# Kernel tuning notes

Hardware: AMD Instinct MI355X
Metric: run time of the kernel (lower is better)

Reference implementation:

```python
import jax, jax.numpy as jnp
import numpy as np

B, T, D, N, L = 8, 2048, 256, 64, 4
LN_EPS = 1e-5


def setup_inputs() -> dict:
    key = jax.random.key(0)
    ks = jax.random.split(key, 8)
    def rn(k, shape, scale=1.0):
        return jax.random.normal(k, shape, dtype=jnp.float32) * scale
    A_init = jnp.log(0.5 + jnp.arange(N, dtype=jnp.float32))  # (N,)
    inp = {
        "sequences": rn(ks[0], (B, T, D)),
        # per-layer stacked params (leading dim L)
        "Wi": rn(ks[1], (L, D, D), 1.0 / np.sqrt(D)),
        "bi": jnp.zeros((L, D), jnp.float32),
        "A_log": jnp.broadcast_to(A_init, (L, D, N)) + 0.0,
        "Cm": rn(ks[2], (L, D, N), 1.0 / np.sqrt(N)),
        "Dp": jnp.ones((L, D), jnp.float32),
        "log_dt": jax.random.uniform(ks[3], (L, D), jnp.float32) * (np.log(0.1) - np.log(0.001)) + np.log(0.001),
        "Wo": rn(ks[4], (L, D, D), 1.0 / np.sqrt(D)),
        "bo": jnp.zeros((L, D), jnp.float32),
        "ln1_g": jnp.ones((L, D), jnp.float32),
        "ln1_b": jnp.zeros((L, D), jnp.float32),
        "ln2_g": jnp.ones((L, D), jnp.float32),
        "ln2_b": jnp.zeros((L, D), jnp.float32),
        "W1": rn(ks[5], (L, D, 4 * D), 1.0 / np.sqrt(D)),
        "b1": jnp.zeros((L, 4 * D), jnp.float32),
        "W2": rn(ks[6], (L, 4 * D, D), 1.0 / np.sqrt(4 * D)),
        "b2": jnp.zeros((L, D), jnp.float32),
        "lnf_g": jnp.ones((D,), jnp.float32),
        "lnf_b": jnp.zeros((D,), jnp.float32),
    }
    return inp


def _ln(x, g, b):
    m = x.mean(-1, keepdims=True)
    v = x.var(-1, keepdims=True)
    return (x - m) / jnp.sqrt(v + LN_EPS) * g + b


def _s4_kernel(A_log_l, Cm_l, log_dt_l, Tlen):
    dt = jnp.exp(log_dt_l)                       # (D,)
    A = -jnp.exp(A_log_l)                        # (D,N)
    A_bar = jnp.exp(A * dt[:, None])             # (D,N)
    B_bar = (A_bar - 1.0) / (A * np.sqrt(N))     # (D,N)
    CB = Cm_l * B_bar                            # (D,N)
    logAb = jnp.log(jnp.clip(A_bar, 1e-10))
    powers = jnp.arange(Tlen, dtype=jnp.float32)
    # (D,N,T) power tensor contracted over N -> (D,T)
    return jnp.einsum('dn,dnt->dt', CB, jnp.exp(logAb[:, :, None] * powers))


def reference(sequences, Wi, bi, A_log, Cm, Dp, log_dt, Wo, bo,
              ln1_g, ln1_b, ln2_g, ln2_b, W1, b1, W2, b2, lnf_g, lnf_b):
    x = sequences  # dropout is identity in eval mode
    Tlen = x.shape[1]
    nfft = 2 * Tlen
    for l in range(L):
        # --- S4D sub-block (pre-norm) ---
        h = _ln(x, ln1_g[l], ln1_b[l])
        u = (h @ Wi[l] + bi[l]).transpose(0, 2, 1)   # (B,D,T)
        K = _s4_kernel(A_log[l], Cm[l], log_dt[l], Tlen)  # (D,T)
        u_f = jnp.fft.rfft(u, n=nfft, axis=-1)
        K_f = jnp.fft.rfft(K, n=nfft, axis=-1)
        y = jnp.fft.irfft(u_f * K_f[None], n=nfft, axis=-1)[..., :Tlen]
        y = y + Dp[l][None, :, None] * u
        y = y.transpose(0, 2, 1) @ Wo[l] + bo[l]
        x = x + y
        # --- MLP sub-block (pre-norm) ---
        h2 = _ln(x, ln2_g[l], ln2_b[l])
        x = x + (jax.nn.gelu(h2 @ W1[l] + b1[l], approximate=False) @ W2[l] + b2[l])
    return _ln(x, lnf_g, lnf_b)
```

## Files before the change

kernel.cpp:

```cpp
#include <hip/hip_runtime.h>
#include <hip/hip_bf16.h>

#define NB 8
#define TT 2048
#define DD 256
#define NN 64
#define LL 4
#define CC 32
#define GG 64
#define BT (NB*TT)

typedef __attribute__((ext_vector_type(8))) short short8;
typedef __attribute__((ext_vector_type(4))) short short4v;
typedef __attribute__((ext_vector_type(4))) float f32x4;

__device__ __forceinline__ float bf2f(__hip_bfloat16 v){ return __bfloat162float(v); }
__device__ __forceinline__ __hip_bfloat16 f2bf(float v){ return __float2bfloat16(v); }
__device__ __forceinline__ short f2bfbits(float v){
  __hip_bfloat16 h = __float2bfloat16(v);
  return __builtin_bit_cast(short, h);
}
__device__ __forceinline__ float bfbits2f(short s){
  __hip_bfloat16 h = __builtin_bit_cast(__hip_bfloat16, s);
  return __bfloat162float(h);
}

#define VMCNT(N) do{ asm volatile("s_waitcnt vmcnt(" #N ")" ::: "memory"); \
                     __builtin_amdgcn_sched_barrier(0); }while(0)
__device__ __forceinline__ void barrier_pre(){
  asm volatile("" ::: "memory");
  __builtin_amdgcn_s_barrier();
  asm volatile("" ::: "memory");
  __builtin_amdgcn_sched_barrier(0);
}
__device__ __forceinline__ void barrier_post(){
  asm volatile("s_waitcnt lgkmcnt(0)" ::: "memory");
  __builtin_amdgcn_sched_barrier(0);
  __builtin_amdgcn_s_barrier();
  asm volatile("" ::: "memory");
  __builtin_amdgcn_sched_barrier(0);
}

__device__ __forceinline__ int get_bf(const void* dtp){
  unsigned u = *(const unsigned*)dtp;
  return ((u >> 16) == (u & 0xFFFFu)) ? 1 : 0;
}

__device__ __forceinline__ float ldin(const void* p, size_t i, int bf){
  return bf ? __bfloat162float(((const __hip_bfloat16*)p)[i]) : ((const float*)p)[i];
}

__device__ __forceinline__ float gelu_f(float x){
  float y = 0.79788456f * fmaf(0.044715f, x*x*x, x);
  float e = __expf(-2.0f * fabsf(y));
  float t = (1.0f - e) / (1.0f + e);
  t = (y >= 0.0f) ? t : -t;
  return 0.5f * x * (1.0f + t);
}

__device__ __forceinline__ void async16(const void* g, void* l){
  __builtin_amdgcn_global_load_lds(
      (const __attribute__((address_space(1))) void*)(unsigned long long)g,
      (__attribute__((address_space(3))) void*)(unsigned long long)l,
      16, 0, 0);
}

__global__ __launch_bounds__(256) void cast_ln_kernel(const void* __restrict__ seq,
    __hip_bfloat16* __restrict__ x, __hip_bfloat16* __restrict__ hN,
    const void* __restrict__ g, const void* __restrict__ b,
    const void* __restrict__ dtp)
{
  int bf = get_bf(dtp);
  int lane = threadIdx.x & 63, w = threadIdx.x >> 6;
  int row = blockIdx.x * 4 + w;
  int c = lane * 4;
  size_t base = (size_t)row*DD + c;
  float v0 = ldin(seq, base+0, bf), v1 = ldin(seq, base+1, bf);
  float v2 = ldin(seq, base+2, bf), v3 = ldin(seq, base+3, bf);
  short4v xk; xk.x=f2bfbits(v0); xk.y=f2bfbits(v1); xk.z=f2bfbits(v2); xk.w=f2bfbits(v3);
  *(short4v*)(x + base) = xk;
  float s = v0+v1+v2+v3;
  #pragma unroll
  for (int o = 1; o < 64; o <<= 1) s += __shfl_xor(s, o);
  float mean = s * (1.0f/DD);
  float d0=v0-mean, d1=v1-mean, d2=v2-mean, d3=v3-mean;
  float sq = d0*d0+d1*d1+d2*d2+d3*d3;
  #pragma unroll
  for (int o = 1; o < 64; o <<= 1) sq += __shfl_xor(sq, o);
  float r = rsqrtf(sq * (1.0f/DD) + 1e-5f);
  short4v hk;
  hk.x = f2bfbits(d0*r*ldin(g,c+0,bf) + ldin(b,c+0,bf));
  hk.y = f2bfbits(d1*r*ldin(g,c+1,bf) + ldin(b,c+1,bf));
  hk.z = f2bfbits(d2*r*ldin(g,c+2,bf) + ldin(b,c+2,bf));
  hk.w = f2bfbits(d3*r*ldin(g,c+3,bf) + ldin(b,c+3,bf));
  *(short4v*)(hN + base) = hk;
}

__global__ __launch_bounds__(256) void transpose_all_kernel(
    const void* __restrict__ Wi, const void* __restrict__ Wo,
    const void* __restrict__ W1, const void* __restrict__ W2,
    __hip_bfloat16* __restrict__ WiT, __hip_bfloat16* __restrict__ WoT,
    __hip_bfloat16* __restrict__ W1T, __hip_bfloat16* __restrict__ W2T,
    const void* __restrict__ dtp)
{
  int bf = get_bf(dtp);
  __shared__ float tile[32][33];
  int id = blockIdx.x;
  const void* W; __hip_bfloat16* Wt; int K, N, l, n0, k0;
  if (id < 256){
    W=Wi; Wt=WiT; K=DD; N=DD;
    int t=id;       l=t>>6; int r=t&63;  n0=(r&7)*32;  k0=(r>>3)*32;
  } else if (id < 512){
    W=Wo; Wt=WoT; K=DD; N=DD;
    int t=id-256;   l=t>>6; int r=t&63;  n0=(r&7)*32;  k0=(r>>3)*32;
  } else if (id < 1536){
    W=W1; Wt=W1T; K=DD; N=4*DD;
    int t=id-512;   l=t>>8; int r=t&255; n0=(r&31)*32; k0=(r>>5)*32;
  } else {
    W=W2; Wt=W2T; K=4*DD; N=DD;
    int t=id-1536;  l=t>>8; int r=t&255; n0=(r&7)*32;  k0=(r>>3)*32;
  }
  size_t zoff = (size_t)l * K * N;
  int tx = threadIdx.x, ty = threadIdx.y;
  #pragma unroll
  for (int i = 0; i < 4; i++)
    tile[ty + i*8][tx] = ldin(W, zoff + (size_t)(k0 + ty + i*8)*N + n0 + tx, bf);
  __syncthreads();
  #pragma unroll
  for (int i = 0; i < 4; i++)
    Wt[zoff + (size_t)(n0 + ty + i*8)*K + k0 + tx] = f2bf(tile[tx][ty + i*8]);
}

__global__ __launch_bounds__(256) void gemm_w1_kernel(
    const __hip_bfloat16* __restrict__ A, const __hip_bfloat16* __restrict__ Wt,
    const void* __restrict__ bias, size_t boff,
    __hip_bfloat16* __restrict__ C, int N, int K, const void* __restrict__ dtp)
{
  int bf = get_bf(dtp);
  __shared__ __align__(16) char smem[49152];
  short (*Als)[2][128][32] = (short(*)[2][128][32])smem;
  short (*Bls)[2][64][32]  = (short(*)[2][64][32])(smem + 32768);
  short* Cls = (short*)smem;
  int tid = threadIdx.x;
  int lane = tid & 63, w = tid >> 6;
  int quad = lane >> 4, row16 = lane & 15;
  int wm = (w >> 1) * 64, wn = (w & 1) * 32;
  int bm = blockIdx.x * 128, bn = blockIdx.y * 64;
  const short* Ag = (const short*)A + (size_t)bm * K;
  const short* Bg = (const short*)Wt + (size_t)bn * K;
  int nt = K >> 6;
  {
    #pragma unroll
    for (int p = 0; p < 4; p++){
      int ch = p*256 + tid; int kc = ch>>9, r=(ch>>2)&127, c=(ch&3)*8;
      async16(Ag + (size_t)r*K + kc*32 + c, &Als[0][kc][r][c]);
    }
    #pragma unroll
    for (int p = 0; p < 2; p++){
      int c2 = p*256 + tid; int k2 = c2>>8, r2=(c2>>2)&63, cc=(c2&3)*8;
      async16(Bg + (size_t)r2*K + k2*32 + cc, &Bls[0][k2][r2][cc]);
    }
  }
  f32x4 acc[4][2] = {};
  for (int t = 0; t < nt; t++){
    int cur = t & 1;
    if (t + 1 < nt){
      int nb_ = cur ^ 1, k0 = (t+1) << 6;
      #pragma unroll
      for (int p = 0; p < 4; p++){
        int ch = p*256 + tid; int kc = ch>>9, r=(ch>>2)&127, c=(ch&3)*8;
        async16(Ag + (size_t)r*K + k0 + kc*32 + c, &Als[nb_][kc][r][c]);
      }
      #pragma unroll
      for (int p = 0; p < 2; p++){
        int c2 = p*256 + tid; int k2 = c2>>8, r2=(c2>>2)&63, cc=(c2&3)*8;
        async16(Bg + (size_t)r2*K + k0 + k2*32 + cc, &Bls[nb_][k2][r2][cc]);
      }
      VMCNT(6);
    } else {
      VMCNT(0);
    }
    barrier_pre();
    #pragma unroll
    for (int kc = 0; kc < 2; kc++){
      short8 af[4], bfr[2];
      #pragma unroll
      for (int i = 0; i < 4; i++)
        af[i] = *(const short8*)&Als[cur][kc][wm + i*16 + row16][quad*8];
      #pragma unroll
      for (int j = 0; j < 2; j++)
        bfr[j] = *(const short8*)&Bls[cur][kc][wn + j*16 + row16][quad*8];
      #pragma unroll
      for (int i = 0; i < 4; i++)
        #pragma unroll
        for (int j = 0; j < 2; j++)
          acc[i][j] = __builtin_amdgcn_mfma_f32_16x16x32_bf16(af[i], bfr[j], acc[i][j], 0, 0, 0);
    }
    barrier_post();
  }
  #pragma unroll
  for (int i = 0; i < 4; i++){
    #pragma unroll
    for (int j = 0; j < 2; j++){
      int col = wn + j*16 + row16;
      float bv = ldin(bias, boff + bn + col, bf);
      #pragma unroll
      for (int r = 0; r < 4; r++){
        int row = wm + i*16 + quad*4 + r;
        Cls[row*72 + col] = f2bfbits(gelu_f(acc[i][j][r] + bv));
      }
    }
  }
  __syncthreads();
  #pragma unroll
  for (int p = 0; p < 4; p++){
    int ch = p*256 + tid;
    int row = ch >> 3, c0 = (ch & 7) * 8;
    short8 v = *(const short8*)&Cls[row*72 + c0];
    *(short8*)&C[(size_t)(bm + row)*N + bn + c0] = v;
  }
}

__global__ __launch_bounds__(256) void gemm_wi_lf_kernel(
    const __hip_bfloat16* __restrict__ A, const __hip_bfloat16* __restrict__ Wt,
    const void* __restrict__ bias, size_t boff,
    __hip_bfloat16* __restrict__ uout, __hip_bfloat16* __restrict__ LFS,
    const float* __restrict__ abT, int K, const void* __restrict__ dtp)
{
  int bf = get_bf(dtp);
  __shared__ __align__(16) char smem[73728];
  short (*Als)[2][32][32]  = (short(*)[2][32][32])smem;
  short (*Bls)[2][256][32] = (short(*)[2][256][32])(smem + 8192);
  float* Cls = (float*)smem;
  int tid = threadIdx.x, lane = tid & 63, w = tid >> 6;
  int quad = lane >> 4, row16 = lane & 15;
  int wn = w * 64;
  int bm = blockIdx.x * 32;
  const short* Ag = (const short*)A + (size_t)bm * K;
  const short* Bg = (const short*)Wt;
  int nt = K >> 6;
  {
    int ch = tid; int kc = ch>>7, r=(ch>>2)&31, c=(ch&3)*8;
    async16(Ag + (size_t)r*K + kc*32 + c, &Als[0][kc][r][c]);
    #pragma unroll
    for (int p = 0; p < 8; p++){
      int c2 = p*256 + tid; int k2 = c2>>10, r2=(c2>>2)&255, cc=(c2&3)*8;
      async16(Bg + (size_t)r2*K + k2*32 + cc, &Bls[0][k2][r2][cc]);
    }
  }
  f32x4 acc[2][4] = {};
  for (int t = 0; t < nt; t++){
    int cur = t & 1;
    if (t + 1 < nt){
      int nb_ = cur ^ 1, k0 = (t+1) << 6;
      int ch = tid; int kc = ch>>7, r=(ch>>2)&31, c=(ch&3)*8;
      async16(Ag + (size_t)r*K + k0 + kc*32 + c, &Als[nb_][kc][r][c]);
      #pragma unroll
      for (int p = 0; p < 8; p++){
        int c2 = p*256 + tid; int k2 = c2>>10, r2=(c2>>2)&255, cc=(c2&3)*8;
        async16(Bg + (size_t)r2*K + k0 + k2*32 + cc, &Bls[nb_][k2][r2][cc]);
      }
      VMCNT(9);
    } else {
      VMCNT(0);
    }
    barrier_pre();
    #pragma unroll
    for (int kc = 0; kc < 2; kc++){
      short8 af[2], bfr[4];
      #pragma unroll
      for (int i = 0; i < 2; i++)
        af[i] = *(const short8*)&Als[cur][kc][i*16 + row16][quad*8];
      #pragma unroll
      for (int j = 0; j < 4; j++)
        bfr[j] = *(const short8*)&Bls[cur][kc][wn + j*16 + row16][quad*8];
      #pragma unroll
      for (int i = 0; i < 2; i++)
        #pragma unroll
        for (int j = 0; j < 4; j++)
          acc[i][j] = __builtin_amdgcn_mfma_f32_16x16x32_bf16(af[i], bfr[j], acc[i][j], 0, 0, 0);
    }
    barrier_post();
  }
  #pragma unroll
  for (int i = 0; i < 2; i++)
    #pragma unroll
    for (int j = 0; j < 4; j++){
      int col = wn + j*16 + row16;
      #pragma unroll
      for (int r = 0; r < 4; r++){
        int row = i*16 + quad*4 + r;
        Cls[row*260 + col] = acc[i][j][r];
      }
    }
  __syncthreads();
  {
    int row = tid >> 3, l7 = tid & 7;
    size_t rbase = (size_t)(bm + row)*DD;
    #pragma unroll
    for (int q = 0; q < 8; q++){
      int c0 = l7*4 + q*32;
      float4 t = *(const float4*)&Cls[row*260 + c0];
      float v0 = t.x + ldin(bias, boff+c0+0, bf);
      float v1 = t.y + ldin(bias, boff+c0+1, bf);
      float v2 = t.z + ldin(bias, boff+c0+2, bf);
      float v3 = t.w + ldin(bias, boff+c0+3, bf);
      float4 wbk; wbk.x=v0; wbk.y=v1; wbk.z=v2; wbk.w=v3;
      *(float4*)&Cls[row*260 + c0] = wbk;
      short4v pk; pk.x=f2bfbits(v0); pk.y=f2bfbits(v1); pk.z=f2bfbits(v2); pk.w=f2bfbits(v3);
      *(short4v*)&uout[rbase + c0] = pk;
    }
  }
  __syncthreads();
  {
    int d = tid;
    int cix = bm >> 5;
    float ab[NN], accn[NN];
    #pragma unroll
    for (int n = 0; n < NN; n++){ ab[n] = abT[n*DD + d]; accn[n] = 0.0f; }
    #pragma unroll 1
    for (int s = 0; s < CC; s++){
      float uv = Cls[s*260 + d];
      #pragma unroll
      for (int n = 0; n < NN; n++) accn[n] = fmaf(ab[n], accn[n], uv);
    }
    #pragma unroll
    for (int n = 0; n < NN; n++)
      LFS[((size_t)cix*NN + n)*DD + d] = f2bf(accn[n]);
  }
}

__global__ __launch_bounds__(256) void s4_scan_kernel(__hip_bfloat16* __restrict__ LFS,
    const float* __restrict__ AbarCT)
{
  int d = threadIdx.x;
  int n = blockIdx.x & (NN-1), b = blockIdx.x >> 6;
  float a = AbarCT[n*DD + d];
  size_t base = ((size_t)(b*GG)*NN + n)*DD + d;
  const size_t gs = (size_t)NN*DD;
  float s = 0.0f;
  #pragma unroll 1
  for (int g = 0; g < GG; g += 4){
    size_t i0 = base + (size_t)(g+0)*gs;
    size_t i1 = base + (size_t)(g+1)*gs;
    size_t i2 = base + (size_t)(g+2)*gs;
    size_t i3 = base + (size_t)(g+3)*gs;
    float lf0 = bf2f(LFS[i0]);
    float lf1 = bf2f(LFS[i1]);
    float lf2 = bf2f(LFS[i2]);
    float lf3 = bf2f(LFS[i3]);
    LFS[i0] = f2bf(s); s = fmaf(a, s, lf0);
    LFS[i1] = f2bf(s); s = fmaf(a, s, lf1);
    LFS[i2] = f2bf(s); s = fmaf(a, s, lf2);
    LFS[i3] = f2bf(s); s = fmaf(a, s, lf3);
  }
}

__global__ __launch_bounds__(512, 4) void gemm_wo_recur_kernel(
    const __hip_bfloat16* __restrict__ uB, const __hip_bfloat16* __restrict__ Sin,
    const float* __restrict__ abT, const float* __restrict__ cbT,
    const void* __restrict__ Dp, size_t dpoff,
    const __hip_bfloat16* __restrict__ Wt, const void* __restrict__ bias, size_t boff,
    const __hip_bfloat16* __restrict__ resx, __hip_bfloat16* __restrict__ xout,
    const void* __restrict__ g, size_t goff, const void* __restrict__ bb, size_t bboff,
    __hip_bfloat16* __restrict__ hout)
{
  int bf = get_bf(Dp);
  __shared__ __align__(16) char smem[50176];
  short* Uls   = (short*)smem;
  short* Afull = (short*)(smem + 16384);
  short* Bext  = (short*)(smem + 32768);
  float* Cls   = (float*)(smem + 16384);
  int tid = threadIdx.x, lane = tid & 63, w = tid >> 6;
  int quad = lane >> 4, row16 = lane & 15;
  int bm = blockIdx.x * CC;
  const short* Bg = (const short*)Wt;
  {
    const short* ug = (const short*)uB + (size_t)bm * DD;
    async16(ug + tid*8,        Uls + tid*8);
    async16(ug + 4096 + tid*8, Uls + 4096 + tid*8);
    #pragma unroll
    for (int p = 0; p < 2; p++){
      int ch = p*512 + tid; int r = ch >> 2, c = (ch & 3) * 8;
      async16(Bg + (size_t)r*DD + c, Bext + ch*8);
    }
  }
  int d = tid >> 1, ng = tid & 1, nb = ng * 32;
  float st[32], ab[32], cb[32];
  {
    const __hip_bfloat16* sbase = Sin + ((size_t)(bm >> 5) * NN + nb)*DD + d;
    const float* abase = abT + (size_t)nb*DD + d;
    const float* cbase = cbT + (size_t)nb*DD + d;
    #pragma unroll
    for (int i = 0; i < 32; i++){
      st[i] = bf2f(sbase[(size_t)i*DD]);
      ab[i] = abase[(size_t)i*DD];
      cb[i] = cbase[(size_t)i*DD];
    }
  }
  float dp = ldin(Dp, dpoff + d, bf);
  __syncthreads();
  {
    short* ya = Afull + (d >> 5)*1024 + (d & 31);
    float uv = bfbits2f(Uls[d]);
    #pragma unroll 1
    for (int tau = 0; tau < CC; tau++){
      float uvn = (tau < CC-1) ? bfbits2f(Uls[(tau+1)*DD + d]) : 0.0f;
      float a0 = 0.0f, a1 = 0.0f, a2 = 0.0f, a3 = 0.0f;
      #pragma unroll
      for (int i = 0; i < 32; i += 4){
        st[i+0] = fmaf(ab[i+0], st[i+0], uv); a0 = fmaf(cb[i+0], st[i+0], a0);
        st[i+1] = fmaf(ab[i+1], st[i+1], uv); a1 = fmaf(cb[i+1], st[i+1], a1);
        st[i+2] = fmaf(ab[i+2], st[i+2], uv); a2 = fmaf(cb[i+2], st[i+2], a2);
        st[i+3] = fmaf(ab[i+3], st[i+3], uv); a3 = fmaf(cb[i+3], st[i+3], a3);
      }
      float tot = (a0 + a1) + (a2 + a3);
      tot += __shfl_xor(tot, 1);
      if (ng == 0) ya[tau*32] = f2bfbits(fmaf(dp, uv, tot));
      uv = uvn;
    }
  }
  __syncthreads();
  int wn = w * 32;
  f32x4 acc[2][2] = {};
  #pragma unroll
  for (int t = 0; t < 8; t++){
    if (t < 7){
      short* nxt = ((t+1) & 1) ? Uls : Bext;
      #pragma unroll
      for (int p = 0; p < 2; p++){
        int ch = p*512 + tid; int r = ch >> 2, c = (ch & 3) * 8;
        async16(Bg + (size_t)r*DD + (t+1)*32 + c, nxt + ch*8);
      }
      VMCNT(2);
    } else {
      VMCNT(0);
    }
    barrier_pre();
    const short* cur = (t & 1) ? Uls : Bext;
    short8 af[2], bfr[2];
    #pragma unroll
    for (int i = 0; i < 2; i++)
      af[i] = *(const short8*)&Afull[t*1024 + (i*16 + row16)*32 + quad*8];
    #pragma unroll
    for (int j = 0; j < 2; j++)
      bfr[j] = *(const short8*)&cur[(wn + j*16 + row16)*32 + quad*8];
    #pragma unroll
    for (int i = 0; i < 2; i++)
      #pragma unroll
      for (int j = 0; j < 2; j++)
        acc[i][j] = __builtin_amdgcn_mfma_f32_16x16x32_bf16(af[i], bfr[j], acc[i][j], 0, 0, 0);
    barrier_post();
  }
  #pragma unroll
  for (int i = 0; i < 2; i++)
    #pragma unroll
    for (int j = 0; j < 2; j++){
      int col = wn + j*16 + row16;
      #pragma unroll
      for (int r = 0; r < 4; r++){
        int row = i*16 + quad*4 + r;
        Cls[row*260 + col] = acc[i][j][r];
      }
    }
  __syncthreads();
  int row = tid >> 4, l4 = tid & 15;
  size_t rbase = (size_t)(bm + row)*DD;
  float v[4][4];
  #pragma unroll
  for (int q = 0; q < 4; q++){
    int c0 = l4*4 + q*64;
    float4 t = *(const float4*)&Cls[row*260 + c0];
    short4v rx = *(const short4v*)&resx[rbase + c0];
    v[q][0] = t.x + ldin(bias, boff+c0+0, bf) + bfbits2f(rx.x);
    v[q][1] = t.y + ldin(bias, boff+c0+1, bf) + bfbits2f(rx.y);
    v[q][2] = t.z + ldin(bias, boff+c0+2, bf) + bfbits2f(rx.z);
    v[q][3] = t.w + ldin(bias, boff+c0+3, bf) + bfbits2f(rx.w);
    short4v pk; pk.x=f2bfbits(v[q][0]); pk.y=f2bfbits(v[q][1]);
    pk.z=f2bfbits(v[q][2]); pk.w=f2bfbits(v[q][3]);
    *(short4v*)&xout[rbase + c0] = pk;
  }
  float s = 0.0f, sq = 0.0f;
  #pragma unroll
  for (int q = 0; q < 4; q++)
    #pragma unroll
    for (int e = 0; e < 4; e++){ s += v[q][e]; sq += v[q][e]*v[q][e]; }
  #pragma unroll
  for (int o = 1; o < 16; o <<= 1){ s += __shfl_xor(s, o); sq += __shfl_xor(sq, o); }
  float mean = s * (1.0f/DD);
  float rstd = rsqrtf(sq * (1.0f/DD) - mean*mean + 1e-5f);
  #pragma unroll
  for (int q = 0; q < 4; q++){
    int c0 = l4*4 + q*64;
    short4v pk;
    pk.x = f2bfbits((v[q][0]-mean)*rstd*ldin(g,goff+c0+0,bf) + ldin(bb,bboff+c0+0,bf));
    pk.y = f2bfbits((v[q][1]-mean)*rstd*ldin(g,goff+c0+1,bf) + ldin(bb,bboff+c0+1,bf));
    pk.z = f2bfbits((v[q][2]-mean)*rstd*ldin(g,goff+c0+2,bf) + ldin(bb,bboff+c0+2,bf));
    pk.w = f2bfbits((v[q][3]-mean)*rstd*ldin(g,goff+c0+3,bf) + ldin(bb,bboff+c0+3,bf));
    *(short4v*)&hout[rbase + c0] = pk;
  }
}

template <int MODE>
__global__ __launch_bounds__(256) void gemm_row_kernel(
    const __hip_bfloat16* __restrict__ A, const __hip_bfloat16* __restrict__ Wt,
    const void* __restrict__ bias, size_t boff,
    const __hip_bfloat16* __restrict__ resx, __hip_bfloat16* __restrict__ xout,
    const void* __restrict__ g, size_t goff,
    const void* __restrict__ bb, size_t bboff,
    __hip_bfloat16* __restrict__ hout, void* __restrict__ vout,
    int K, const void* __restrict__ dtp)
{
  int bf = get_bf(dtp);
  __shared__ __align__(16) char smem[73728];
  short (*Als)[2][32][32]  = (short(*)[2][32][32])smem;
  short (*Bls)[2][256][32] = (short(*)[2][256][32])(smem + 8192);
  float* Cls = (float*)smem;
  int tid = threadIdx.x, lane = tid & 63, w = tid >> 6;
  int quad = lane >> 4, row16 = lane & 15;
  int wn = w * 64;
  int bm = blockIdx.x * 32;
  const short* Ag = (const short*)A + (size_t)bm * K;
  const short* Bg = (const short*)Wt;
  int nt = K >> 6;
  {
    int ch = tid; int kc = ch>>7, r=(ch>>2)&31, c=(ch&3)*8;
    async16(Ag + (size_t)r*K + kc*32 + c, &Als[0][kc][r][c]);
    #pragma unroll
    for (int p = 0; p < 8; p++){
      int c2 = p*256 + tid; int k2 = c2>>10, r2=(c2>>2)&255, cc=(c2&3)*8;
      async16(Bg + (size_t)r2*K + k2*32 + cc, &Bls[0][k2][r2][cc]);
    }
  }
  f32x4 acc[2][4] = {};
  for (int t = 0; t < nt; t++){
    int cur = t & 1;
    if (t + 1 < nt){
      int nb_ = cur ^ 1, k0 = (t+1) << 6;
      int ch = tid; int kc = ch>>7, r=(ch>>2)&31, c=(ch&3)*8;
      async16(Ag + (size_t)r*K + k0 + kc*32 + c, &Als[nb_][kc][r][c]);
      #pragma unroll
      for (int p = 0; p < 8; p++){
        int c2 = p*256 + tid; int k2 = c2>>10, r2=(c2>>2)&255, cc=(c2&3)*8;
        async16(Bg + (size_t)r2*K + k0 + k2*32 + cc, &Bls[nb_][k2][r2][cc]);
      }
      VMCNT(9);
    } else {
      VMCNT(0);
    }
    barrier_pre();
    #pragma unroll
    for (int kc = 0; kc < 2; kc++){
      short8 af[2], bfr[4];
      #pragma unroll
      for (int i = 0; i < 2; i++)
        af[i] = *(const short8*)&Als[cur][kc][i*16 + row16][quad*8];
      #pragma unroll
      for (int j = 0; j < 4; j++)
        bfr[j] = *(const short8*)&Bls[cur][kc][wn + j*16 + row16][quad*8];
      #pragma unroll
      for (int i = 0; i < 2; i++)
        #pragma unroll
        for (int j = 0; j < 4; j++)
          acc[i][j] = __builtin_amdgcn_mfma_f32_16x16x32_bf16(af[i], bfr[j], acc[i][j], 0, 0, 0);
    }
    barrier_post();
  }
  #pragma unroll
  for (int i = 0; i < 2; i++)
    #pragma unroll
    for (int j = 0; j < 4; j++){
      int col = wn + j*16 + row16;
      #pragma unroll
      for (int r = 0; r < 4; r++){
        int row = i*16 + quad*4 + r;
        Cls[row*260 + col] = acc[i][j][r];
      }
    }
  __syncthreads();
  int row = tid >> 3, l7 = tid & 7;
  size_t rbase = (size_t)(bm + row)*DD;
  float v[8][4];
  #pragma unroll
  for (int q = 0; q < 8; q++){
    int c0 = l7*4 + q*32;
    float4 t = *(const float4*)&Cls[row*260 + c0];
    short4v rx = *(const short4v*)&resx[rbase + c0];
    v[q][0] = t.x + ldin(bias, boff+c0+0, bf) + bfbits2f(rx.x);
    v[q][1] = t.y + ldin(bias, boff+c0+1, bf) + bfbits2f(rx.y);
    v[q][2] = t.z + ldin(bias, boff+c0+2, bf) + bfbits2f(rx.z);
    v[q][3] = t.w + ldin(bias, boff+c0+3, bf) + bfbits2f(rx.w);
    if (MODE == 1){
      short4v pk; pk.x=f2bfbits(v[q][0]); pk.y=f2bfbits(v[q][1]);
      pk.z=f2bfbits(v[q][2]); pk.w=f2bfbits(v[q][3]);
      *(short4v*)&xout[rbase + c0] = pk;
    }
  }
  float s = 0.0f, sq = 0.0f;
  #pragma unroll
  for (int q = 0; q < 8; q++)
    #pragma unroll
    for (int e = 0; e < 4; e++){ s += v[q][e]; sq += v[q][e]*v[q][e]; }
  #pragma unroll
  for (int o = 1; o < 8; o <<= 1){ s += __shfl_xor(s, o); sq += __shfl_xor(sq, o); }
  float mean = s * (1.0f/DD);
  float rstd = rsqrtf(sq * (1.0f/DD) - mean*mean + 1e-5f);
  #pragma unroll
  for (int q = 0; q < 8; q++){
    int c0 = l7*4 + q*32;
    float o0 = (v[q][0]-mean)*rstd*ldin(g,goff+c0+0,bf) + ldin(bb,bboff+c0+0,bf);
    float o1 = (v[q][1]-mean)*rstd*ldin(g,goff+c0+1,bf) + ldin(bb,bboff+c0+1,bf);
    float o2 = (v[q][2]-mean)*rstd*ldin(g,goff+c0+2,bf) + ldin(bb,bboff+c0+2,bf);
    float o3 = (v[q][3]-mean)*rstd*ldin(g,goff+c0+3,bf) + ldin(bb,bboff+c0+3,bf);
    if (MODE == 1){
      short4v pk; pk.x=f2bfbits(o0); pk.y=f2bfbits(o1); pk.z=f2bfbits(o2); pk.w=f2bfbits(o3);
      *(short4v*)&hout[rbase + c0] = pk;
    } else {
      if (bf){
        short4v pk; pk.x=f2bfbits(o0); pk.y=f2bfbits(o1); pk.z=f2bfbits(o2); pk.w=f2bfbits(o3);
        *(short4v*)&((__hip_bfloat16*)vout)[rbase + c0] = pk;
      } else {
        float4 pk; pk.x=o0; pk.y=o1; pk.z=o2; pk.w=o3;
        *(float4*)&((float*)vout)[rbase + c0] = pk;
      }
    }
  }
}

__global__ __launch_bounds__(256) void s4_setup_kernel(const void* __restrict__ A_log,
    const void* __restrict__ Cm, const void* __restrict__ log_dt,
    float* __restrict__ AbarT, float* __restrict__ AbarCT, float* __restrict__ cbT,
    const void* __restrict__ dtp)
{
  int bf = get_bf(dtp);
  int d = threadIdx.x, n = blockIdx.x, l = blockIdx.y;
  float dtv = expf(ldin(log_dt, (size_t)l*DD + d, bf));
  float A   = -expf(ldin(A_log, ((size_t)l*DD + d)*NN + n, bf));
  float ab  = expf(A * dtv);
  float bbv = (fabsf(A) > 1e-8f) ? (ab - 1.0f) / (A * 8.0f) : dtv * 0.125f;
  float cb  = ldin(Cm, ((size_t)l*DD + d)*NN + n, bf) * bbv;
  size_t o = ((size_t)l*NN + n)*DD + d;
  AbarT[o] = ab;
  cbT[o]   = cb;
  float p = ab;
  #pragma unroll
  for (int i = 0; i < 5; i++) p *= p;
  AbarCT[o] = p;
}

extern "C" void kernel_launch(void* const* d_in, const int* in_sizes, int n_in,
                              void* d_out, int out_size, void* d_ws, size_t ws_size,
                              hipStream_t stream) {
  const void* seq   = d_in[0];
  const void* Wi    = d_in[1];
  const void* bi    = d_in[2];
  const void* A_log = d_in[3];
  const void* Cm    = d_in[4];
  const void* Dp    = d_in[5];
  const void* logdt = d_in[6];
  const void* Wo    = d_in[7];
  const void* bo    = d_in[8];
  const void* ln1g  = d_in[9];
  const void* ln1b  = d_in[10];
  const void* ln2g  = d_in[11];
  const void* ln2b  = d_in[12];
  const void* W1    = d_in[13];
  const void* b1    = d_in[14];
  const void* W2    = d_in[15];
  const void* b2    = d_in[16];
  const void* lnfg  = d_in[17];
  const void* lnfb  = d_in[18];

  char* ws = (char*)d_ws;
  size_t off = 0;
  __hip_bfloat16* x   = (__hip_bfloat16*)(ws + off); off += (size_t)BT*DD*2;
  __hip_bfloat16* uB  = (__hip_bfloat16*)(ws + off); off += (size_t)BT*DD*2;
  __hip_bfloat16* hN  = (__hip_bfloat16*)(ws + off); off += (size_t)BT*DD*2;
  __hip_bfloat16* mid = (__hip_bfloat16*)(ws + off); off += (size_t)BT*4*DD*2;
  __hip_bfloat16* LFS = (__hip_bfloat16*)(ws + off); off += (size_t)NB*GG*NN*DD*2;
  __hip_bfloat16* WiT = (__hip_bfloat16*)(ws + off); off += (size_t)LL*DD*DD*2;
  __hip_bfloat16* WoT = (__hip_bfloat16*)(ws + off); off += (size_t)LL*DD*DD*2;
  __hip_bfloat16* W1T = (__hip_bfloat16*)(ws + off); off += (size_t)LL*DD*4*DD*2;
  __hip_bfloat16* W2T = (__hip_bfloat16*)(ws + off); off += (size_t)LL*4*DD*DD*2;
  float* AbarT  = (float*)(ws + off); off += (size_t)LL*NN*DD*4;
  float* AbarCT = (float*)(ws + off); off += (size_t)LL*NN*DD*4;
  float* cbT    = (float*)(ws + off); off += (size_t)LL*NN*DD*4;

  (void)in_sizes; (void)n_in; (void)out_size; (void)ws_size;

  cast_ln_kernel<<<BT/4, 256, 0, stream>>>(seq, x, hN, ln1g, ln1b, Dp);
  transpose_all_kernel<<<2560, dim3(32,8), 0, stream>>>(
      Wi, Wo, W1, W2, WiT, WoT, W1T, W2T, Dp);
  s4_setup_kernel<<<dim3(NN, LL), DD, 0, stream>>>(A_log, Cm, logdt, AbarT, AbarCT, cbT, Dp);

  for (int l = 0; l < LL; l++){
    const size_t oD  = (size_t)l*DD;
    const size_t o4D = (size_t)l*4*DD;
    const float* abT  = AbarT  + (size_t)l*NN*DD;
    const float* abCT = AbarCT + (size_t)l*NN*DD;
    const float* cbTl = cbT    + (size_t)l*NN*DD;

    gemm_wi_lf_kernel<<<BT/32, 256, 0, stream>>>(
        hN, WiT + (size_t)l*DD*DD, bi, oD, uB, LFS, abT, DD, Dp);
    s4_scan_kernel<<<NB*NN, 256, 0, stream>>>(LFS, abCT);
    gemm_wo_recur_kernel<<<BT/32, 512, 0, stream>>>(
        uB, LFS, abT, cbTl, Dp, oD,
        WoT + (size_t)l*DD*DD, bo, oD, x, x,
        ln2g, oD, ln2b, oD, hN);

    gemm_w1_kernel<<<dim3(BT/128, 4*DD/64), 256, 0, stream>>>(
        hN, W1T + (size_t)l*DD*4*DD, b1, o4D, mid, 4*DD, DD, Dp);
    if (l < LL-1){
      gemm_row_kernel<1><<<BT/32, 256, 0, stream>>>(
          mid, W2T + (size_t)l*4*DD*DD, b2, oD, x, x,
          ln1g, (size_t)(l+1)*DD, ln1b, (size_t)(l+1)*DD, hN, nullptr, 4*DD, Dp);
    } else {
      gemm_row_kernel<2><<<BT/32, 256, 0, stream>>>(
          mid, W2T + (size_t)l*4*DD*DD, b2, oD, x, nullptr,
          lnfg, 0, lnfb, 0, nullptr, d_out, 4*DD, Dp);
    }
  }
}
```

Before: 589.0 us.

## Double threads in Wo recurrence kernel to split state over four lanes

Launches gemm_wo_recur_kernel with 1024 threads instead of 512. Each channel's 64-state recurrence is now split across four lanes of 16 states each, with an extra shuffle reduction. The MFMA tiling is remapped so 16 waves each compute a 16x32 output tile, and the loads and LayerNorm epilogue are redistributed to match. The goal is to shorten the serial per-thread recurrence and use more waves per block. In exchange there are more shuffles, and the 1024-thread block with __launch_bounds__(1024,4) may be limited by occupancy and register pressure.

Result: slower. 646.8 us (+9.8%).

```diff
diff --git a/kernel.cpp b/kernel.cpp
--- a/kernel.cpp
+++ b/kernel.cpp
@@ -356,7 +356,7 @@
   }
 }
 
-__global__ __launch_bounds__(512, 4) void gemm_wo_recur_kernel(
+__global__ __launch_bounds__(1024, 4) void gemm_wo_recur_kernel(
     const __hip_bfloat16* __restrict__ uB, const __hip_bfloat16* __restrict__ Sin,
     const float* __restrict__ abT, const float* __restrict__ cbT,
     const void* __restrict__ Dp, size_t dpoff,
@@ -377,22 +377,18 @@
   const short* Bg = (const short*)Wt;
   {
     const short* ug = (const short*)uB + (size_t)bm * DD;
-    async16(ug + tid*8,        Uls + tid*8);
-    async16(ug + 4096 + tid*8, Uls + 4096 + tid*8);
-    #pragma unroll
-    for (int p = 0; p < 2; p++){
-      int ch = p*512 + tid; int r = ch >> 2, c = (ch & 3) * 8;
-      async16(Bg + (size_t)r*DD + c, Bext + ch*8);
-    }
-  }
-  int d = tid >> 1, ng = tid & 1, nb = ng * 32;
-  float st[32], ab[32], cb[32];
+    async16(ug + tid*8, Uls + tid*8);
+    int r = tid >> 2, c = (tid & 3) * 8;
+    async16(Bg + (size_t)r*DD + c, Bext + tid*8);
+  }
+  int d = tid >> 2, ng = tid & 3, nb = ng * 16;
+  float st[16], ab[16], cb[16];
   {
     const __hip_bfloat16* sbase = Sin + ((size_t)(bm >> 5) * NN + nb)*DD + d;
     const float* abase = abT + (size_t)nb*DD + d;
     const float* cbase = cbT + (size_t)nb*DD + d;
     #pragma unroll
-    for (int i = 0; i < 32; i++){
+    for (int i = 0; i < 16; i++){
       st[i] = bf2f(sbase[(size_t)i*DD]);
       ab[i] = abase[(size_t)i*DD];
       cb[i] = cbase[(size_t)i*DD];
@@ -408,7 +404,7 @@
       float uvn = (tau < CC-1) ? bfbits2f(Uls[(tau+1)*DD + d]) : 0.0f;
       float a0 = 0.0f, a1 = 0.0f, a2 = 0.0f, a3 = 0.0f;
       #pragma unroll
-      for (int i = 0; i < 32; i += 4){
+      for (int i = 0; i < 16; i += 4){
         st[i+0] = fmaf(ab[i+0], st[i+0], uv); a0 = fmaf(cb[i+0], st[i+0], a0);
         st[i+1] = fmaf(ab[i+1], st[i+1], uv); a1 = fmaf(cb[i+1], st[i+1], a1);
         st[i+2] = fmaf(ab[i+2], st[i+2], uv); a2 = fmaf(cb[i+2], st[i+2], a2);
@@ -416,60 +412,52 @@
       }
       float tot = (a0 + a1) + (a2 + a3);
       tot += __shfl_xor(tot, 1);
+      tot += __shfl_xor(tot, 2);
       if (ng == 0) ya[tau*32] = f2bfbits(fmaf(dp, uv, tot));
       uv = uvn;
     }
   }
   __syncthreads();
-  int wn = w * 32;
-  f32x4 acc[2][2] = {};
+  int wm = (w >> 3) * 16, wn = (w & 7) * 32;
+  f32x4 acc[2] = {};
   #pragma unroll
   for (int t = 0; t < 8; t++){
     if (t < 7){
       short* nxt = ((t+1) & 1) ? Uls : Bext;
-      #pragma unroll
-      for (int p = 0; p < 2; p++){
-        int ch = p*512 + tid; int r = ch >> 2, c = (ch & 3) * 8;
-        async16(Bg + (size_t)r*DD + (t+1)*32 + c, nxt + ch*8);
-      }
-      VMCNT(2);
+      int r = tid >> 2, c = (tid & 3) * 8;
+      async16(Bg + (size_t)r*DD + (t+1)*32 + c, nxt + tid*8);
+      VMCNT(1);
     } else {
       VMCNT(0);
     }
     barrier_pre();
     const short* cur = (t & 1) ? Uls : Bext;
-    short8 af[2], bfr[2];
-    #pragma unroll
-    for (int i = 0; i < 2; i++)
-      af[i] = *(const short8*)&Afull[t*1024 + (i*16 + row16)*32 + quad*8];
+    short8 af = *(const short8*)&Afull[t*1024 + (wm + row16)*32 + quad*8];
+    short8 bfr[2];
     #pragma unroll
     for (int j = 0; j < 2; j++)
       bfr[j] = *(const short8*)&cur[(wn + j*16 + row16)*32 + quad*8];
     #pragma unroll
-    for (int i = 0; i < 2; i++)
-      #pragma unroll
-      for (int j = 0; j < 2; j++)
-        acc[i][j] = __builtin_amdgcn_mfma_f32_16x16x32_bf16(af[i], bfr[j], acc[i][j], 0, 0, 0);
+    for (int j = 0; j < 2; j++)
+      acc[j] = __builtin_amdgcn_mfma_f32_16x16x32_bf16(af, bfr[j], acc[j], 0, 0, 0);
     barrier_post();
   }
   #pragma unroll
-  for (int i = 0; i < 2; i++)
-    #pragma unroll
-    for (int j = 0; j < 2; j++){
-      int col = wn + j*16 + row16;
-      #pragma unroll
-      for (int r = 0; r < 4; r++){
-        int row = i*16 + quad*4 + r;
-        Cls[row*260 + col] = acc[i][j][r];
-      }
-    }
+  for (int j = 0; j < 2; j++){
+    int col = wn + j*16 + row16;
+    #pragma unroll
+    for (int r = 0; r < 4; r++){
+      int row = wm + quad*4 + r;
+      Cls[row*260 + col] = acc[j][r];
+    }
+  }
   __syncthreads();
-  int row = tid >> 4, l4 = tid & 15;
+  int row = tid >> 5, l5 = tid & 31;
   size_t rbase = (size_t)(bm + row)*DD;
-  float v[4][4];
-  #pragma unroll
-  for (int q = 0; q < 4; q++){
-    int c0 = l4*4 + q*64;
+  float v[2][4];
+  #pragma unroll
+  for (int q = 0; q < 2; q++){
+    int c0 = l5*4 + q*128;
     float4 t = *(const float4*)&Cls[row*260 + c0];
     short4v rx = *(const short4v*)&resx[rbase + c0];
     v[q][0] = t.x + ldin(bias, boff+c0+0, bf) + bfbits2f(rx.x);
@@ -482,16 +470,16 @@
   }
   float s = 0.0f, sq = 0.0f;
   #pragma unroll
-  for (int q = 0; q < 4; q++)
+  for (int q = 0; q < 2; q++)
     #pragma unroll
     for (int e = 0; e < 4; e++){ s += v[q][e]; sq += v[q][e]*v[q][e]; }
   #pragma unroll
-  for (int o = 1; o < 16; o <<= 1){ s += __shfl_xor(s, o); sq += __shfl_xor(sq, o); }
+  for (int o = 1; o < 32; o <<= 1){ s += __shfl_xor(s, o); sq += __shfl_xor(sq, o); }
   float mean = s * (1.0f/DD);
   float rstd = rsqrtf(sq * (1.0f/DD) - mean*mean + 1e-5f);
   #pragma unroll
-  for (int q = 0; q < 4; q++){
-    int c0 = l4*4 + q*64;
+  for (int q = 0; q < 2; q++){
+    int c0 = l5*4 + q*128;
     short4v pk;
     pk.x = f2bfbits((v[q][0]-mean)*rstd*ldin(g,goff+c0+0,bf) + ldin(bb,bboff+c0+0,bf));
     pk.y = f2bfbits((v[q][1]-mean)*rstd*ldin(g,goff+c0+1,bf) + ldin(bb,bboff+c0+1,bf));
@@ -703,7 +691,7 @@
     gemm_wi_lf_kernel<<<BT/32, 256, 0, stream>>>(
         hN, WiT + (size_t)l*DD*DD, bi, oD, uB, LFS, abT, DD, Dp);
     s4_scan_kernel<<<NB*NN, 256, 0, stream>>>(LFS, abCT);
-    gemm_wo_recur_kernel<<<BT/32, 512, 0, stream>>>(
+    gemm_wo_recur_kernel<<<BT/32, 1024, 0, stream>>>(
         uB, LFS, abT, cbTl, Dp, oD,
         WoT + (size_t)l*DD*DD, bo, oD, x, x,
         ln2g, oD, ln2b, oD, hN);
```
